# Performance work log

Measured on AMD Instinct MI355X. Metric: run time of the kernel, lower is better.

## Reference

```python
import jax, jax.numpy as jnp
import numpy as np

B, T, E = 16, 512, 768
N_ANN = 32                      # mentions per passage
N_ENT = B * N_ANN               # 512 flat entities, each 2E wide
P = B * N_ANN * (N_ANN - 1)     # 15872 ordered pairs
H = 512                          # MLP hidden size (head_args layer_sizes)
ENTITY_DIM = 256                 # relation MLP output = 2*entity_dim
D4 = 4 * E                       # relation_input width


def setup_inputs() -> dict:
    key = jax.random.key(0)
    ks = jax.random.split(key, 14)
    inp = {
        "x": jax.random.normal(ks[0], (B, T, E), dtype=jnp.float32),
        "src_tokens": jax.random.randint(ks[1], (B, T), 0, 32000),
        "mask_annotation": jax.random.randint(ks[2], (B, T), 0, 2),
        "all_annotations": jax.random.randint(ks[3], (B, 2 * N_ANN), 0, T),
        "n_annotations": N_ANN,
        "relation_entity_indices_left": jax.random.randint(ks[4], (P,), 0, N_ENT),
        "relation_entity_indices_right": jax.random.randint(ks[5], (P,), 0, N_ENT),
        # relation MLP: Linear(4E,H) -> ReLU -> Linear(H, 2*entity_dim)
        "W1": jax.random.normal(ks[6], (D4, H), dtype=jnp.float32) / np.sqrt(D4),
        "b1": jnp.zeros((H,), dtype=jnp.float32),
        "W2": jax.random.normal(ks[7], (H, 2 * ENTITY_DIM), dtype=jnp.float32) / np.sqrt(H),
        "b2": jnp.zeros((2 * ENTITY_DIM,), dtype=jnp.float32),
        # score MLP: Linear(4E,H) -> ReLU -> Linear(H, 1)
        "Ws1": jax.random.normal(ks[8], (D4, H), dtype=jnp.float32) / np.sqrt(D4),
        "bs1": jnp.zeros((H,), dtype=jnp.float32),
        "Ws2": jax.random.normal(ks[9], (H, 1), dtype=jnp.float32) / np.sqrt(H),
        "bs2": jnp.zeros((1,), dtype=jnp.float32),
    }
    return inp


def reference(x, src_tokens, mask_annotation, all_annotations, n_annotations,
              relation_entity_indices_left, relation_entity_indices_right,
              W1, b1, W2, b2, Ws1, bs1, Ws2, bs2):
    batch_size, _, enc_dim = x.shape
    # idx_repeated: each batch row repeated 2*n_annotations times
    idx_rep = jnp.repeat(jnp.arange(batch_size), 2 * n_annotations)
    ann_flat = all_annotations.reshape(-1)
    # gather annotation tokens -> [B*2n, E] -> pairwise concat [B*n, 2E]
    ent_tokens = x[idx_rep, ann_flat]
    entity_representation = ent_tokens.reshape(-1, 2 * enc_dim)
    left = entity_representation[relation_entity_indices_left]
    right = entity_representation[relation_entity_indices_right]
    relation_input = jnp.concatenate((left, right), axis=-1)  # [P, 4E]
    h_rel = jax.nn.relu(relation_input @ W1 + b1)
    relation_representation = h_rel @ W2 + b2                 # [P, 2*entity_dim]
    h_sc = jax.nn.relu(relation_input @ Ws1 + bs1)
    relation_score = jnp.abs((h_sc @ Ws2 + bs2).squeeze(-1))  # [P]
    return entity_representation, relation_representation, relation_score
```

## Files before the change

kernel.cpp:

```cpp
#include <hip/hip_runtime.h>

typedef unsigned short u16;
typedef __attribute__((ext_vector_type(8))) short short8;
typedef __attribute__((ext_vector_type(4))) float floatx4;

#define N_ENT   512
#define P_PAIRS 15872
#define E_DIM   768
#define D2      1536
#define OUT_ENT   (512*1536)
#define OUT_REL   (15872*512)

#define BM 128
#define BN 128
#define BK 32

__device__ __forceinline__ u16 f2bf(float f){
    union { float f; unsigned u; } v; v.f = f;
    unsigned r = v.u + 0x7fffu + ((v.u >> 16) & 1u);
    return (u16)(r >> 16);
}

__global__ void transpose_k(const float* __restrict__ src, u16* __restrict__ dst,
                            int R, int C) {
    __shared__ float tile[32][33];
    const int bx = blockIdx.x * 32;
    const int by = blockIdx.y * 32;
    const int tx = threadIdx.x, ty = threadIdx.y;
#pragma unroll
    for (int i = 0; i < 32; i += 8)
        tile[ty + i][tx] = src[(size_t)(by + ty + i) * C + bx + tx];
    __syncthreads();
#pragma unroll
    for (int i = 0; i < 32; i += 8)
        dst[(size_t)(bx + ty + i) * R + by + tx] = f2bf(tile[tx][ty + i]);
}

__global__ void gather_k(const float* __restrict__ x, const int* __restrict__ ann,
                         float* __restrict__ entF, u16* __restrict__ entB) {
    const int e = blockIdx.x;
    const int t = threadIdx.x;
    const int half = t / 192;
    const int chunk = t % 192;
    const int tok = ann[e * 2 + half];
    const int b = e >> 5;
    const float4 v = ((const float4*)(x + (size_t)(b * 512 + tok) * E_DIM))[chunk];
    ((float4*)(entF + (size_t)e * D2 + half * E_DIM))[chunk] = v;
    ushort4 o;
    o.x = f2bf(v.x); o.y = f2bf(v.y); o.z = f2bf(v.z); o.w = f2bf(v.w);
    ((ushort4*)(entB + (size_t)e * D2 + half * E_DIM))[chunk] = o;
}

__global__ __launch_bounds__(256)
void gemm_uv(const u16* __restrict__ Ent, const u16* __restrict__ W1T,
             const u16* __restrict__ Ws1T, float* __restrict__ UV) {
    __shared__ __align__(16) u16 As[BM * BK];
    __shared__ __align__(16) u16 Bs[BN * BK];
    const int t = threadIdx.x;
    const int m0 = blockIdx.x * BM;
    const int n0g = blockIdx.y * BN;
    const int g = n0g >> 9;
    const int n0 = n0g & 511;
    const u16* WT = (g < 2) ? W1T : Ws1T;
    const int koff = (g & 1) * D2;

    const int wave = t >> 6, lane = t & 63;
    const int wm = (wave >> 1) * 64, wn = (wave & 1) * 64;
    const int l15 = lane & 15, quad = lane >> 4;
    const int srow = t >> 2;
    const int soff = (t & 3) * 8;

    floatx4 acc[4][4] = {};
    for (int k0 = 0; k0 < D2; k0 += BK) {
        uint4 a0 = *(const uint4*)(Ent + (size_t)(m0 + srow) * D2 + k0 + soff);
        uint4 a1 = *(const uint4*)(Ent + (size_t)(m0 + 64 + srow) * D2 + k0 + soff);
        uint4 b0 = *(const uint4*)(WT + (size_t)(n0 + srow) * 3072 + koff + k0 + soff);
        uint4 b1 = *(const uint4*)(WT + (size_t)(n0 + 64 + srow) * 3072 + koff + k0 + soff);
        __syncthreads();
        *(uint4*)(As + srow * BK + soff) = a0;
        *(uint4*)(As + (64 + srow) * BK + soff) = a1;
        *(uint4*)(Bs + srow * BK + soff) = b0;
        *(uint4*)(Bs + (64 + srow) * BK + soff) = b1;
        __syncthreads();
        short8 af[4], bfr[4];
#pragma unroll
        for (int i = 0; i < 4; i++) {
            af[i]  = *(const short8*)(As + (wm + i * 16 + l15) * BK + quad * 8);
            bfr[i] = *(const short8*)(Bs + (wn + i * 16 + l15) * BK + quad * 8);
        }
#pragma unroll
        for (int i = 0; i < 4; i++)
#pragma unroll
            for (int j = 0; j < 4; j++)
                acc[i][j] = __builtin_amdgcn_mfma_f32_16x16x32_bf16(af[i], bfr[j], acc[i][j], 0, 0, 0);
    }
    float* outg = UV + (size_t)g * (512 * 512);
#pragma unroll
    for (int j = 0; j < 4; j++) {
        const int col = n0 + wn + j * 16 + l15;
#pragma unroll
        for (int i = 0; i < 4; i++) {
            const int rowb = m0 + wm + i * 16 + quad * 4;
#pragma unroll
            for (int r = 0; r < 4; r++)
                outg[(size_t)(rowb + r) * 512 + col] = acc[i][j][r];
        }
    }
}

__global__ __launch_bounds__(256)
void pair_k(const float* __restrict__ UV, const int* __restrict__ left,
            const int* __restrict__ right, const float* __restrict__ b1,
            const float* __restrict__ bs1, const float* __restrict__ Ws2,
            const float* __restrict__ bs2, u16* __restrict__ Hrel,
            float* __restrict__ score) {
    const int p = blockIdx.x * 4 + (threadIdx.x >> 6);
    const int lane = threadIdx.x & 63;
    const int l = left[p], r = right[p];
    const float* U  = UV + (size_t)l * 512;
    const float* V  = UV + 1 * 262144 + (size_t)r * 512;
    const float* Us = UV + 2 * 262144 + (size_t)l * 512;
    const float* Vs = UV + 3 * 262144 + (size_t)r * 512;
    float acc = 0.f;
#pragma unroll
    for (int s = 0; s < 8; s++) {
        const int k = lane + s * 64;
        float h = U[k] + V[k] + b1[k];
        Hrel[(size_t)p * 512 + k] = f2bf(fmaxf(h, 0.f));
        float hs = Us[k] + Vs[k] + bs1[k];
        acc += fmaxf(hs, 0.f) * Ws2[k];
    }
#pragma unroll
    for (int off = 32; off; off >>= 1) acc += __shfl_down(acc, off, 64);
    if (lane == 0) score[p] = fabsf(acc + bs2[0]);
}

__global__ __launch_bounds__(256)
void gemm_rel(const u16* __restrict__ A, const u16* __restrict__ BT,
              const float* __restrict__ b2, float* __restrict__ Cout) {
    __shared__ __align__(16) u16 As[BM * BK];
    __shared__ __align__(16) u16 Bs[BN * BK];
    const int t = threadIdx.x;
    const int m0 = blockIdx.x * BM;
    const int n0 = blockIdx.y * BN;
    const int wave = t >> 6, lane = t & 63;
    const int wm = (wave >> 1) * 64, wn = (wave & 1) * 64;
    const int l15 = lane & 15, quad = lane >> 4;
    const int srow = t >> 2;
    const int soff = (t & 3) * 8;

    floatx4 acc[4][4] = {};
    for (int k0 = 0; k0 < 512; k0 += BK) {
        uint4 a0 = *(const uint4*)(A + (size_t)(m0 + srow) * 512 + k0 + soff);
        uint4 a1 = *(const uint4*)(A + (size_t)(m0 + 64 + srow) * 512 + k0 + soff);
        uint4 b0 = *(const uint4*)(BT + (size_t)(n0 + srow) * 512 + k0 + soff);
        uint4 b1v = *(const uint4*)(BT + (size_t)(n0 + 64 + srow) * 512 + k0 + soff);
        __syncthreads();
        *(uint4*)(As + srow * BK + soff) = a0;
        *(uint4*)(As + (64 + srow) * BK + soff) = a1;
        *(uint4*)(Bs + srow * BK + soff) = b0;
        *(uint4*)(Bs + (64 + srow) * BK + soff) = b1v;
        __syncthreads();
        short8 af[4], bfr[4];
#pragma unroll
        for (int i = 0; i < 4; i++) {
            af[i]  = *(const short8*)(As + (wm + i * 16 + l15) * BK + quad * 8);
            bfr[i] = *(const short8*)(Bs + (wn + i * 16 + l15) * BK + quad * 8);
        }
#pragma unroll
        for (int i = 0; i < 4; i++)
#pragma unroll
            for (int j = 0; j < 4; j++)
                acc[i][j] = __builtin_amdgcn_mfma_f32_16x16x32_bf16(af[i], bfr[j], acc[i][j], 0, 0, 0);
    }
#pragma unroll
    for (int j = 0; j < 4; j++) {
        const int col = n0 + wn + j * 16 + l15;
        const float bias = b2[col];
#pragma unroll
        for (int i = 0; i < 4; i++) {
            const int rowb = m0 + wm + i * 16 + quad * 4;
#pragma unroll
            for (int r = 0; r < 4; r++)
                Cout[(size_t)(rowb + r) * 512 + col] = acc[i][j][r] + bias;
        }
    }
}

extern "C" void kernel_launch(void* const* d_in, const int* in_sizes, int n_in,
                              void* d_out, int out_size, void* d_ws, size_t ws_size,
                              hipStream_t stream) {
    const float* x   = (const float*)d_in[0];
    const int* ann   = (const int*)d_in[3];
    const int* left  = (const int*)d_in[5];
    const int* right = (const int*)d_in[6];
    const float* W1  = (const float*)d_in[7];
    const float* b1  = (const float*)d_in[8];
    const float* W2  = (const float*)d_in[9];
    const float* b2  = (const float*)d_in[10];
    const float* Ws1 = (const float*)d_in[11];
    const float* bs1 = (const float*)d_in[12];
    const float* Ws2 = (const float*)d_in[13];
    const float* bs2 = (const float*)d_in[14];

    float* out = (float*)d_out;
    float* entF = out;
    float* rel  = out + OUT_ENT;
    float* sco  = out + OUT_ENT + OUT_REL;

    u16* W1T  = (u16*)d_ws;
    u16* Ws1T = W1T + 512 * 3072;
    u16* W2T  = Ws1T + 512 * 3072;
    u16* EntB = W2T + 512 * 512;
    float* UV = (float*)(EntB + 512 * 1536);
    u16* Hrel = (u16*)(UV + 4 * 512 * 512);

    transpose_k<<<dim3(16, 96), dim3(32, 8), 0, stream>>>(W1, W1T, 3072, 512);
    transpose_k<<<dim3(16, 96), dim3(32, 8), 0, stream>>>(Ws1, Ws1T, 3072, 512);
    transpose_k<<<dim3(16, 16), dim3(32, 8), 0, stream>>>(W2, W2T, 512, 512);
    gather_k<<<512, 384, 0, stream>>>(x, ann, entF, EntB);
    gemm_uv<<<dim3(4, 16), 256, 0, stream>>>(EntB, W1T, Ws1T, UV);
    pair_k<<<P_PAIRS / 4, 256, 0, stream>>>(UV, left, right, b1, bs1, Ws2, bs2, Hrel, sco);
    gemm_rel<<<dim3(124, 4), 256, 0, stream>>>(Hrel, W2T, b2, rel);
}
```

Baseline: 175.0 us.

## Fuse prep kernels, retile UV GEMM with async LDS loads, fuse pair into rel GEMM

The three weight transposes and the entity gather are merged into one prep kernel. The UV GEMM switches to 64x64 tiles with 256 blocks, up from 64, and loads tiles through global_load_lds. The pair kernel is folded into the relation GEMM, which builds the ReLU hidden rows on the fly from U/V, so the bf16 Hrel intermediate is never written or read. Score blocks run in the same launch. This cuts launch count and Hrel traffic, but the GEMM's A-operand now does per-row gather loads from UV inside the k-loop.

After: 165.5 us. 5.4% less time.

```diff
diff --git a/kernel.cpp b/kernel.cpp
--- a/kernel.cpp
+++ b/kernel.cpp
@@ -4,102 +4,116 @@
 typedef __attribute__((ext_vector_type(8))) short short8;
 typedef __attribute__((ext_vector_type(4))) float floatx4;
 
-#define N_ENT   512
 #define P_PAIRS 15872
 #define E_DIM   768
 #define D2      1536
 #define OUT_ENT   (512*1536)
 #define OUT_REL   (15872*512)
 
-#define BM 128
-#define BN 128
-#define BK 32
-
 __device__ __forceinline__ u16 f2bf(float f){
     union { float f; unsigned u; } v; v.f = f;
     unsigned r = v.u + 0x7fffu + ((v.u >> 16) & 1u);
     return (u16)(r >> 16);
 }
-
-__global__ void transpose_k(const float* __restrict__ src, u16* __restrict__ dst,
-                            int R, int C) {
-    __shared__ float tile[32][33];
-    const int bx = blockIdx.x * 32;
-    const int by = blockIdx.y * 32;
-    const int tx = threadIdx.x, ty = threadIdx.y;
-#pragma unroll
-    for (int i = 0; i < 32; i += 8)
-        tile[ty + i][tx] = src[(size_t)(by + ty + i) * C + bx + tx];
-    __syncthreads();
-#pragma unroll
-    for (int i = 0; i < 32; i += 8)
-        dst[(size_t)(bx + ty + i) * R + by + tx] = f2bf(tile[tx][ty + i]);
-}
-
-__global__ void gather_k(const float* __restrict__ x, const int* __restrict__ ann,
-                         float* __restrict__ entF, u16* __restrict__ entB) {
-    const int e = blockIdx.x;
+__device__ __forceinline__ unsigned pack2(float a, float b){
+    return (unsigned)f2bf(a) | ((unsigned)f2bf(b) << 16);
+}
+__device__ __forceinline__ void async_ld16(const void* g, void* lds_base){
+    __builtin_amdgcn_global_load_lds(
+        (const __attribute__((address_space(1))) unsigned*)g,
+        (__attribute__((address_space(3))) unsigned*)lds_base, 16, 0, 0);
+}
+
+__global__ __launch_bounds__(256)
+void prep_k(const float* __restrict__ W1, const float* __restrict__ Ws1,
+            const float* __restrict__ W2, const float* __restrict__ x,
+            const int* __restrict__ ann,
+            u16* __restrict__ W1T, u16* __restrict__ Ws1T, u16* __restrict__ W2T,
+            float* __restrict__ entF, u16* __restrict__ entB) {
+    const int bid = blockIdx.x;
     const int t = threadIdx.x;
-    const int half = t / 192;
-    const int chunk = t % 192;
-    const int tok = ann[e * 2 + half];
-    const int b = e >> 5;
-    const float4 v = ((const float4*)(x + (size_t)(b * 512 + tok) * E_DIM))[chunk];
-    ((float4*)(entF + (size_t)e * D2 + half * E_DIM))[chunk] = v;
-    ushort4 o;
-    o.x = f2bf(v.x); o.y = f2bf(v.y); o.z = f2bf(v.z); o.w = f2bf(v.w);
-    ((ushort4*)(entB + (size_t)e * D2 + half * E_DIM))[chunk] = o;
+    if (bid < 3328) {
+        __shared__ float tile[32][33];
+        const float* src; u16* dst; int R, C, b;
+        if (bid < 1536)      { src = W1;  dst = W1T;  R = 3072; C = 512; b = bid; }
+        else if (bid < 3072) { src = Ws1; dst = Ws1T; R = 3072; C = 512; b = bid - 1536; }
+        else                 { src = W2;  dst = W2T;  R = 512;  C = 512; b = bid - 3072; }
+        const int bx = (b & 15) * 32;
+        const int by = (b >> 4) * 32;
+        const int tx = t & 31, ty = t >> 5;
+#pragma unroll
+        for (int i = 0; i < 32; i += 8)
+            tile[ty + i][tx] = src[(size_t)(by + ty + i) * C + bx + tx];
+        __syncthreads();
+#pragma unroll
+        for (int i = 0; i < 32; i += 8)
+            dst[(size_t)(bx + ty + i) * R + by + tx] = f2bf(tile[tx][ty + i]);
+    } else {
+        const int e = bid - 3328;
+#pragma unroll
+        for (int pass = 0; pass < 2; pass++) {
+            const int c = t + pass * 256;
+            if (c >= 384) break;
+            const int half = c / 192;
+            const int tok = ann[e * 2 + half];
+            const int b = e >> 5;
+            const float4 v = ((const float4*)(x + (size_t)(b * 512 + tok) * E_DIM))[c % 192];
+            ((float4*)(entF + (size_t)e * D2))[c] = v;
+            uint2 o; o.x = pack2(v.x, v.y); o.y = pack2(v.z, v.w);
+            ((uint2*)(entB + (size_t)e * D2))[c] = o;
+        }
+    }
 }
 
 __global__ __launch_bounds__(256)
 void gemm_uv(const u16* __restrict__ Ent, const u16* __restrict__ W1T,
              const u16* __restrict__ Ws1T, float* __restrict__ UV) {
-    __shared__ __align__(16) u16 As[BM * BK];
-    __shared__ __align__(16) u16 Bs[BN * BK];
+    __shared__ __align__(16) u16 As[64 * 32];
+    __shared__ __align__(16) u16 Bs[64 * 32];
     const int t = threadIdx.x;
-    const int m0 = blockIdx.x * BM;
-    const int n0g = blockIdx.y * BN;
+    const int bid = blockIdx.x;
+    const int m0 = (bid & 7) * 64;
+    const int n0g = (bid >> 3) * 64;
     const int g = n0g >> 9;
     const int n0 = n0g & 511;
     const u16* WT = (g < 2) ? W1T : Ws1T;
     const int koff = (g & 1) * D2;
 
     const int wave = t >> 6, lane = t & 63;
-    const int wm = (wave >> 1) * 64, wn = (wave & 1) * 64;
+    const int wm = (wave >> 1) * 32, wn = (wave & 1) * 32;
     const int l15 = lane & 15, quad = lane >> 4;
     const int srow = t >> 2;
-    const int soff = (t & 3) * 8;
-
-    floatx4 acc[4][4] = {};
-    for (int k0 = 0; k0 < D2; k0 += BK) {
-        uint4 a0 = *(const uint4*)(Ent + (size_t)(m0 + srow) * D2 + k0 + soff);
-        uint4 a1 = *(const uint4*)(Ent + (size_t)(m0 + 64 + srow) * D2 + k0 + soff);
-        uint4 b0 = *(const uint4*)(WT + (size_t)(n0 + srow) * 3072 + koff + k0 + soff);
-        uint4 b1 = *(const uint4*)(WT + (size_t)(n0 + 64 + srow) * 3072 + koff + k0 + soff);
+    const int sk = (t & 3) * 8;
+
+    const u16* gA = Ent + (size_t)(m0 + srow) * D2 + sk;
+    const u16* gB = WT + (size_t)(n0 + srow) * 3072 + koff + sk;
+    u16* lA = As + wave * 512;
+    u16* lB = Bs + wave * 512;
+
+    floatx4 acc[2][2] = {};
+    for (int k0 = 0; k0 < D2; k0 += 32) {
         __syncthreads();
-        *(uint4*)(As + srow * BK + soff) = a0;
-        *(uint4*)(As + (64 + srow) * BK + soff) = a1;
-        *(uint4*)(Bs + srow * BK + soff) = b0;
-        *(uint4*)(Bs + (64 + srow) * BK + soff) = b1;
+        async_ld16(gA + k0, lA);
+        async_ld16(gB + k0, lB);
         __syncthreads();
-        short8 af[4], bfr[4];
-#pragma unroll
-        for (int i = 0; i < 4; i++) {
-            af[i]  = *(const short8*)(As + (wm + i * 16 + l15) * BK + quad * 8);
-            bfr[i] = *(const short8*)(Bs + (wn + i * 16 + l15) * BK + quad * 8);
-        }
-#pragma unroll
-        for (int i = 0; i < 4; i++)
-#pragma unroll
-            for (int j = 0; j < 4; j++)
-                acc[i][j] = __builtin_amdgcn_mfma_f32_16x16x32_bf16(af[i], bfr[j], acc[i][j], 0, 0, 0);
-    }
-    float* outg = UV + (size_t)g * (512 * 512);
-#pragma unroll
-    for (int j = 0; j < 4; j++) {
+        short8 af[2], bf[2];
+#pragma unroll
+        for (int i = 0; i < 2; i++) {
+            af[i] = *(const short8*)(As + (wm + i * 16 + l15) * 32 + quad * 8);
+            bf[i] = *(const short8*)(Bs + (wn + i * 16 + l15) * 32 + quad * 8);
+        }
+#pragma unroll
+        for (int i = 0; i < 2; i++)
+#pragma unroll
+            for (int j = 0; j < 2; j++)
+                acc[i][j] = __builtin_amdgcn_mfma_f32_16x16x32_bf16(af[i], bf[j], acc[i][j], 0, 0, 0);
+    }
+    float* outg = UV + (size_t)g * 262144;
+#pragma unroll
+    for (int j = 0; j < 2; j++) {
         const int col = n0 + wn + j * 16 + l15;
 #pragma unroll
-        for (int i = 0; i < 4; i++) {
+        for (int i = 0; i < 2; i++) {
             const int rowb = m0 + wm + i * 16 + quad * 4;
 #pragma unroll
             for (int r = 0; r < 4; r++)
@@ -109,80 +123,126 @@
 }
 
 __global__ __launch_bounds__(256)
-void pair_k(const float* __restrict__ UV, const int* __restrict__ left,
-            const int* __restrict__ right, const float* __restrict__ b1,
-            const float* __restrict__ bs1, const float* __restrict__ Ws2,
-            const float* __restrict__ bs2, u16* __restrict__ Hrel,
-            float* __restrict__ score) {
-    const int p = blockIdx.x * 4 + (threadIdx.x >> 6);
-    const int lane = threadIdx.x & 63;
-    const int l = left[p], r = right[p];
-    const float* U  = UV + (size_t)l * 512;
-    const float* V  = UV + 1 * 262144 + (size_t)r * 512;
-    const float* Us = UV + 2 * 262144 + (size_t)l * 512;
-    const float* Vs = UV + 3 * 262144 + (size_t)r * 512;
-    float acc = 0.f;
-#pragma unroll
-    for (int s = 0; s < 8; s++) {
-        const int k = lane + s * 64;
-        float h = U[k] + V[k] + b1[k];
-        Hrel[(size_t)p * 512 + k] = f2bf(fmaxf(h, 0.f));
-        float hs = Us[k] + Vs[k] + bs1[k];
-        acc += fmaxf(hs, 0.f) * Ws2[k];
-    }
-#pragma unroll
-    for (int off = 32; off; off >>= 1) acc += __shfl_down(acc, off, 64);
-    if (lane == 0) score[p] = fabsf(acc + bs2[0]);
-}
-
-__global__ __launch_bounds__(256)
-void gemm_rel(const u16* __restrict__ A, const u16* __restrict__ BT,
-              const float* __restrict__ b2, float* __restrict__ Cout) {
-    __shared__ __align__(16) u16 As[BM * BK];
-    __shared__ __align__(16) u16 Bs[BN * BK];
+void rel_score_k(const float* __restrict__ UV, const int* __restrict__ left,
+                 const int* __restrict__ right, const float* __restrict__ b1,
+                 const float* __restrict__ bs1, const float* __restrict__ Ws2,
+                 const float* __restrict__ bs2, const u16* __restrict__ W2T,
+                 const float* __restrict__ b2, float* __restrict__ rel,
+                 float* __restrict__ score) {
+    const int bid = blockIdx.x;
     const int t = threadIdx.x;
-    const int m0 = blockIdx.x * BM;
-    const int n0 = blockIdx.y * BN;
     const int wave = t >> 6, lane = t & 63;
-    const int wm = (wave >> 1) * 64, wn = (wave & 1) * 64;
-    const int l15 = lane & 15, quad = lane >> 4;
-    const int srow = t >> 2;
-    const int soff = (t & 3) * 8;
-
-    floatx4 acc[4][4] = {};
-    for (int k0 = 0; k0 < 512; k0 += BK) {
-        uint4 a0 = *(const uint4*)(A + (size_t)(m0 + srow) * 512 + k0 + soff);
-        uint4 a1 = *(const uint4*)(A + (size_t)(m0 + 64 + srow) * 512 + k0 + soff);
-        uint4 b0 = *(const uint4*)(BT + (size_t)(n0 + srow) * 512 + k0 + soff);
-        uint4 b1v = *(const uint4*)(BT + (size_t)(n0 + 64 + srow) * 512 + k0 + soff);
-        __syncthreads();
-        *(uint4*)(As + srow * BK + soff) = a0;
-        *(uint4*)(As + (64 + srow) * BK + soff) = a1;
-        *(uint4*)(Bs + srow * BK + soff) = b0;
-        *(uint4*)(Bs + (64 + srow) * BK + soff) = b1v;
-        __syncthreads();
-        short8 af[4], bfr[4];
-#pragma unroll
-        for (int i = 0; i < 4; i++) {
-            af[i]  = *(const short8*)(As + (wm + i * 16 + l15) * BK + quad * 8);
-            bfr[i] = *(const short8*)(Bs + (wn + i * 16 + l15) * BK + quad * 8);
-        }
-#pragma unroll
-        for (int i = 0; i < 4; i++)
-#pragma unroll
-            for (int j = 0; j < 4; j++)
-                acc[i][j] = __builtin_amdgcn_mfma_f32_16x16x32_bf16(af[i], bfr[j], acc[i][j], 0, 0, 0);
-    }
-#pragma unroll
-    for (int j = 0; j < 4; j++) {
-        const int col = n0 + wn + j * 16 + l15;
-        const float bias = b2[col];
-#pragma unroll
-        for (int i = 0; i < 4; i++) {
-            const int rowb = m0 + wm + i * 16 + quad * 4;
-#pragma unroll
-            for (int r = 0; r < 4; r++)
-                Cout[(size_t)(rowb + r) * 512 + col] = acc[i][j][r] + bias;
+
+    if (bid < 496) {
+        __shared__ __align__(16) u16 As[128 * 32];
+        __shared__ __align__(16) u16 Bs[128 * 32];
+        const int m0 = (bid >> 2) * 128;
+        const int n0 = (bid & 3) * 128;
+        const int wm = (wave >> 1) * 64, wn = (wave & 1) * 64;
+        const int l15 = lane & 15, quad = lane >> 4;
+
+        const int arow = t >> 1;
+        const int koff16 = (t & 1) * 16;
+        const int li = left[m0 + arow], ri = right[m0 + arow];
+        const float4* Up = (const float4*)(UV + (size_t)li * 512 + koff16);
+        const float4* Vp = (const float4*)(UV + 262144 + (size_t)ri * 512 + koff16);
+        const float4* B1 = (const float4*)(b1 + koff16);
+        const int brow = t >> 2;
+        const int bk = (t & 3) * 8;
+        const u16* gB0 = W2T + (size_t)(n0 + brow) * 512 + bk;
+        const u16* gB1 = W2T + (size_t)(n0 + 64 + brow) * 512 + bk;
+        u16* lB0 = Bs + wave * 512;
+        u16* lB1 = Bs + 2048 + wave * 512;
+        uint4* aDst = (uint4*)(As + t * 16);
+
+        floatx4 acc[4][4] = {};
+        for (int k0 = 0; k0 < 512; k0 += 32) {
+            float4 uu[4], vv[4], bb[4];
+            const int kq = k0 >> 2;
+#pragma unroll
+            for (int j = 0; j < 4; j++) {
+                uu[j] = Up[kq + j]; vv[j] = Vp[kq + j]; bb[j] = B1[kq + j];
+            }
+            __syncthreads();
+            async_ld16(gB0 + k0, lB0);
+            async_ld16(gB1 + k0, lB1);
+            uint4 h0, h1;
+            {
+                float4 h;
+                h.x = fmaxf(uu[0].x + vv[0].x + bb[0].x, 0.f);
+                h.y = fmaxf(uu[0].y + vv[0].y + bb[0].y, 0.f);
+                h.z = fmaxf(uu[0].z + vv[0].z + bb[0].z, 0.f);
+                h.w = fmaxf(uu[0].w + vv[0].w + bb[0].w, 0.f);
+                h0.x = pack2(h.x, h.y); h0.y = pack2(h.z, h.w);
+                h.x = fmaxf(uu[1].x + vv[1].x + bb[1].x, 0.f);
+                h.y = fmaxf(uu[1].y + vv[1].y + bb[1].y, 0.f);
+                h.z = fmaxf(uu[1].z + vv[1].z + bb[1].z, 0.f);
+                h.w = fmaxf(uu[1].w + vv[1].w + bb[1].w, 0.f);
+                h0.z = pack2(h.x, h.y); h0.w = pack2(h.z, h.w);
+                h.x = fmaxf(uu[2].x + vv[2].x + bb[2].x, 0.f);
+                h.y = fmaxf(uu[2].y + vv[2].y + bb[2].y, 0.f);
+                h.z = fmaxf(uu[2].z + vv[2].z + bb[2].z, 0.f);
+                h.w = fmaxf(uu[2].w + vv[2].w + bb[2].w, 0.f);
+                h1.x = pack2(h.x, h.y); h1.y = pack2(h.z, h.w);
+                h.x = fmaxf(uu[3].x + vv[3].x + bb[3].x, 0.f);
+                h.y = fmaxf(uu[3].y + vv[3].y + bb[3].y, 0.f);
+                h.z = fmaxf(uu[3].z + vv[3].z + bb[3].z, 0.f);
+                h.w = fmaxf(uu[3].w + vv[3].w + bb[3].w, 0.f);
+                h1.z = pack2(h.x, h.y); h1.w = pack2(h.z, h.w);
+            }
+            aDst[0] = h0; aDst[1] = h1;
+            __syncthreads();
+            short8 af[4], bf[4];
+#pragma unroll
+            for (int i = 0; i < 4; i++) {
+                af[i] = *(const short8*)(As + (wm + i * 16 + l15) * 32 + quad * 8);
+                bf[i] = *(const short8*)(Bs + (wn + i * 16 + l15) * 32 + quad * 8);
+            }
+#pragma unroll
+            for (int i = 0; i < 4; i++)
+#pragma unroll
+                for (int j = 0; j < 4; j++)
+                    acc[i][j] = __builtin_amdgcn_mfma_f32_16x16x32_bf16(af[i], bf[j], acc[i][j], 0, 0, 0);
+        }
+#pragma unroll
+        for (int j = 0; j < 4; j++) {
+            const int col = n0 + wn + j * 16 + l15;
+            const float bias = b2[col];
+#pragma unroll
+            for (int i = 0; i < 4; i++) {
+                const int rowb = m0 + wm + i * 16 + quad * 4;
+#pragma unroll
+                for (int r = 0; r < 4; r++)
+                    rel[(size_t)(rowb + r) * 512 + col] = acc[i][j][r] + bias;
+            }
+        }
+    } else {
+        const int pid0 = (bid - 496) * 32 + wave * 8;
+        const float4* Wsp = (const float4*)(Ws2 + lane * 8);
+        const float4* Bsp = (const float4*)(bs1 + lane * 8);
+        const float4 w0 = Wsp[0], w1 = Wsp[1];
+        const float4 s0 = Bsp[0], s1 = Bsp[1];
+        const float bias = bs2[0];
+#pragma unroll
+        for (int it = 0; it < 8; it++) {
+            const int p = pid0 + it;
+            const int l = left[p], r = right[p];
+            const float4* us = (const float4*)(UV + 2 * 262144 + (size_t)l * 512 + lane * 8);
+            const float4* vs = (const float4*)(UV + 3 * 262144 + (size_t)r * 512 + lane * 8);
+            const float4 a0 = us[0], a1 = us[1];
+            const float4 c0 = vs[0], c1 = vs[1];
+            float acc;
+            acc  = fmaxf(a0.x + c0.x + s0.x, 0.f) * w0.x;
+            acc += fmaxf(a0.y + c0.y + s0.y, 0.f) * w0.y;
+            acc += fmaxf(a0.z + c0.z + s0.z, 0.f) * w0.z;
+            acc += fmaxf(a0.w + c0.w + s0.w, 0.f) * w0.w;
+            acc += fmaxf(a1.x + c1.x + s1.x, 0.f) * w1.x;
+            acc += fmaxf(a1.y + c1.y + s1.y, 0.f) * w1.y;
+            acc += fmaxf(a1.z + c1.z + s1.z, 0.f) * w1.z;
+            acc += fmaxf(a1.w + c1.w + s1.w, 0.f) * w1.w;
+#pragma unroll
+            for (int off = 32; off; off >>= 1) acc += __shfl_down(acc, off, 64);
+            if (lane == 0) score[p] = fabsf(acc + bias);
         }
     }
 }
@@ -213,13 +273,8 @@
     u16* W2T  = Ws1T + 512 * 3072;
     u16* EntB = W2T + 512 * 512;
     float* UV = (float*)(EntB + 512 * 1536);
-    u16* Hrel = (u16*)(UV + 4 * 512 * 512);
-
-    transpose_k<<<dim3(16, 96), dim3(32, 8), 0, stream>>>(W1, W1T, 3072, 512);
-    transpose_k<<<dim3(16, 96), dim3(32, 8), 0, stream>>>(Ws1, Ws1T, 3072, 512);
-    transpose_k<<<dim3(16, 16), dim3(32, 8), 0, stream>>>(W2, W2T, 512, 512);
-    gather_k<<<512, 384, 0, stream>>>(x, ann, entF, EntB);
-    gemm_uv<<<dim3(4, 16), 256, 0, stream>>>(EntB, W1T, Ws1T, UV);
-    pair_k<<<P_PAIRS / 4, 256, 0, stream>>>(UV, left, right, b1, bs1, Ws2, bs2, Hrel, sco);
-    gemm_rel<<<dim3(124, 4), 256, 0, stream>>>(Hrel, W2T, b2, rel);
-}
+
+    prep_k<<<3840, 256, 0, stream>>>(W1, Ws1, W2, x, ann, W1T, Ws1T, W2T, entF, EntB);
+    gemm_uv<<<256, 256, 0, stream>>>(EntB, W1T, Ws1T, UV);
+    rel_score_k<<<992, 256, 0, stream>>>(UV, left, right, b1, bs1, Ws2, bs2, W2T, b2, rel, sco);
+}
```
